# Kernel optimization log

Measured on AMD Instinct MI355X. Metric: run time of the kernel, lower is better.

The kernel has to match this reference:

```python
import jax, jax.numpy as jnp
import numpy as np

B, N, S, K = 8, 4096, 256, 128   # clouds, points/cloud, FPS samples (num_vote_test), neighbor cap
R = 0.2                           # ball-query radius
M = 45                            # FoldingNet grid side -> 45*45 = 2025 grid points


def _fps(pos):
    """Deterministic farthest point sampling of S points from pos [N,3] (start at index 0)."""
    n = pos.shape[0]
    big = jnp.finfo(pos.dtype).max

    def step(carry, _):
        mind, last = carry
        d = jnp.sum((pos - pos[last]) ** 2, axis=-1)
        mind = jnp.minimum(mind, d)
        nxt = jnp.argmax(mind).astype(jnp.int32)
        return (mind, nxt), nxt

    init = (jnp.full((n,), big, pos.dtype), jnp.int32(0))
    _, rest = jax.lax.scan(step, init, None, length=S - 1)
    return jnp.concatenate([jnp.zeros((1,), jnp.int32), rest])


def _forward(pos, Wt, bt, Wc1, bc1, Wc2, bc2, Wc3, bc3, We1, be1, We2, be2,
             Wf11, bf11, Wf12, bf12, Wf13, bf13, Wf21, bf21, Wf22, bf22, Wf23, bf23):
    lrelu = jax.nn.leaky_relu  # slope 0.01, matches torch LeakyReLU default
    # transformer: mlp([3,64]) -- BatchNorm at eval with default stats is identity
    x = lrelu(pos @ Wt + bt)                                  # [B,N,64]
    # FPS per cloud
    idx = jax.vmap(_fps)(pos)                                  # [B,S]
    new_pos = jnp.take_along_axis(pos, idx[..., None], axis=1)  # [B,S,3]
    # radius ball query: first K in-ball neighbors by index order (torch_cluster semantics)
    d2 = jnp.sum((new_pos[:, :, None, :] - pos[:, None, :, :]) ** 2, -1)  # [B,S,N]
    inball = d2 <= R * R
    keep = inball & (jnp.cumsum(inball, axis=-1) <= K)
    order = jnp.where(keep, jnp.arange(N)[None, None, :], N)
    nidx = jnp.sort(order, axis=-1)[..., :K]                   # [B,S,K]
    valid = nidx < N
    nsafe = jnp.minimum(nidx, N - 1)
    gather = jax.vmap(lambda a, i: a[i])
    xj = gather(x, nsafe)                                      # [B,S,K,64]
    pj = gather(pos, nsafe)                                    # [B,S,K,3]
    # PointConv: mlp(cat[x_j, pos_j - pos_i]) with max aggregation
    feat = jnp.concatenate([xj, pj - new_pos[:, :, None, :]], -1)  # [B,S,K,67]
    h = lrelu(feat @ Wc1 + bc1)
    h = lrelu(h @ Wc2 + bc2)
    h = lrelu(h @ Wc3 + bc3)                                   # [B,S,K,512]
    neg = jnp.finfo(h.dtype).min
    agg = jnp.max(jnp.where(valid[..., None], h, neg), axis=2)  # [B,S,512]
    # encoder mlp([515, 512, 2*bottleneck], last=True)
    e = lrelu(jnp.concatenate([agg, new_pos], -1) @ We1 + be1)
    e = e @ We2 + be2                                          # [B,S,2*bottleneck]
    mean, logvar = jnp.split(e, 2, axis=-1)
    std = jnp.exp(0.5 * logvar)
    # feature_selection (eval, rand=False): all S votes contribute; vote aggregation
    z = jnp.sum(mean / std, axis=1) / jnp.sum(1.0 / std, axis=1)  # [B,bottleneck]
    # FoldingNet decoder: 45x45 grid in [-0.3,0.3]^2, conv1x1 == last-dim linear
    g1 = np.linspace(-0.3, 0.3, M, dtype=np.float32)
    mg = np.meshgrid(g1, g1)
    grid = jnp.asarray(np.stack([mg[0].reshape(-1), mg[1].reshape(-1)], -1))  # [M*M,2]
    G = M * M
    code = jnp.broadcast_to(z[:, None, :], (z.shape[0], G, z.shape[1]))
    gb = jnp.broadcast_to(grid[None], (z.shape[0], G, 2))
    f = jnp.concatenate([code, gb], -1)                        # [B,G,bottleneck+2]
    f = jax.nn.relu(f @ Wf11 + bf11)
    f = jax.nn.relu(f @ Wf12 + bf12)
    f = f @ Wf13 + bf13                                        # [B,G,3]
    f2 = jnp.concatenate([code, f], -1)                        # [B,G,bottleneck+3]
    f2 = jax.nn.relu(f2 @ Wf21 + bf21)
    f2 = jax.nn.relu(f2 @ Wf22 + bf22)
    return f2 @ Wf23 + bf23                                    # [B,G,3]


_PARAM_SHAPES = [
    ("Wt", (3, 64)), ("bt", (64,)),
    ("Wc1", (67, 64)), ("bc1", (64,)),
    ("Wc2", (64, 128)), ("bc2", (128,)),
    ("Wc3", (128, 512)), ("bc3", (512,)),
    ("We1", (515, 512)), ("be1", (512,)),
    ("We2", (512, 2048)), ("be2", (2048,)),
    ("Wf11", (1026, 512)), ("bf11", (512,)),
    ("Wf12", (512, 512)), ("bf12", (512,)),
    ("Wf13", (512, 3)), ("bf13", (3,)),
    ("Wf21", (1027, 512)), ("bf21", (512,)),
    ("Wf22", (512, 512)), ("bf22", (512,)),
    ("Wf23", (512, 3)), ("bf23", (3,)),
]


def setup_inputs() -> dict:
    key = jax.random.key(0)
    inp = {"pos": jax.random.uniform(key, (B, N, 3), jnp.float32)}
    for i, (nm, sh) in enumerate(_PARAM_SHAPES):
        k = jax.random.fold_in(key, i + 1)
        fan_in = sh[0]
        inp[nm] = jax.random.normal(k, sh, jnp.float32) / np.sqrt(fan_in)
    return inp


def reference(pos, Wt, bt, Wc1, bc1, Wc2, bc2, Wc3, bc3, We1, be1, We2, be2,
              Wf11, bf11, Wf12, bf12, Wf13, bf13, Wf21, bf21, Wf22, bf22, Wf23, bf23):
    return _forward(pos, Wt, bt, Wc1, bc1, Wc2, bc2, Wc3, bc3, We1, be1, We2, be2,
                    Wf11, bf11, Wf12, bf12, Wf13, bf13, Wf21, bf21, Wf22, bf22, Wf23, bf23)
```

## Files before the change

kernel.cpp:

```cpp
#include <hip/hip_runtime.h>
#include <math.h>

#define BATCH 8
#define NPTS 4096
#define SSAMP 256
#define KNBR 128
#define GGRID 2025

typedef __attribute__((ext_vector_type(8))) short bf16x8;
typedef __attribute__((ext_vector_type(8))) unsigned short u16x8;
typedef __attribute__((ext_vector_type(4))) float f32x4;
#define MFMA16(a, b, c) __builtin_amdgcn_mfma_f32_16x16x32_bf16((a), (b), (c), 0, 0, 0)

__device__ __forceinline__ float lrelu01(float v) { return v > 0.f ? v : 0.01f * v; }
__device__ __forceinline__ unsigned short f2bf(float f) {
    unsigned u = __float_as_uint(f);
    unsigned r = (u + 0x7FFFu + ((u >> 16) & 1u)) >> 16;
    return (unsigned short)r;
}
__device__ __forceinline__ unsigned long long umax64(unsigned long long a, unsigned long long b) {
    return a > b ? a : b;
}

__global__ void preconv_kernel(const float* __restrict__ Wc1, const float* __restrict__ Wc2,
                               const float* __restrict__ Wc3, const float* __restrict__ We1,
                               const float* __restrict__ We2, const float* __restrict__ Wf12,
                               const float* __restrict__ Wf22,
                               unsigned short* __restrict__ W1T, unsigned short* __restrict__ W2T,
                               unsigned short* __restrict__ W3T, unsigned short* __restrict__ We1T,
                               unsigned short* __restrict__ We2T, unsigned short* __restrict__ Wf12T,
                               unsigned short* __restrict__ Wf22T) {
    int o = blockIdx.x * 256 + threadIdx.x;
    const int S1 = 6144, S2 = 8192, S3 = 65536, S4 = 294912, S5 = 1048576, S6 = 262144;
    if (o < S1) { int n = o / 96, k = o - n * 96; W1T[o] = f2bf(k < 67 ? Wc1[k * 64 + n] : 0.f); return; }
    o -= S1;
    if (o < S2) { int n = o >> 6, k = o & 63; W2T[o] = f2bf(Wc2[k * 128 + n]); return; }
    o -= S2;
    if (o < S3) { int n = o >> 7, k = o & 127; W3T[o] = f2bf(Wc3[k * 512 + n]); return; }
    o -= S3;
    if (o < S4) { int n = o / 576, k = o - n * 576; We1T[o] = f2bf(k < 515 ? We1[k * 512 + n] : 0.f); return; }
    o -= S4;
    if (o < S5) {
        int np = o >> 9, k = o & 511;
        int src = (np & 1) ? 1024 + (np >> 1) : (np >> 1);
        We2T[o] = f2bf(We2[(size_t)k * 2048 + src]);
        return;
    }
    o -= S5;
    if (o < S6) { int n = o >> 9, k = o & 511; Wf12T[o] = f2bf(Wf12[k * 512 + n]); return; }
    o -= S6;
    { int n = o >> 9, k = o & 511; Wf22T[o] = f2bf(Wf22[k * 512 + n]); }
}

__global__ void __launch_bounds__(256, 3) stage1_kernel(
    const float* __restrict__ pos, float* __restrict__ newpos, int* __restrict__ prog,
    const float* __restrict__ Wt, const float* __restrict__ bt,
    const unsigned short* __restrict__ W1T, const unsigned short* __restrict__ W2T,
    const unsigned short* __restrict__ W3T,
    const float* __restrict__ bc1, const float* __restrict__ bc2, const float* __restrict__ bc3,
    unsigned short* __restrict__ encin) {
    __shared__ __align__(16) unsigned char smem[53760];
    int blk = blockIdx.x, t = threadIdx.x;
    int wave = t >> 6, lane = t & 63;

    if (blk < 8) {
        float* pxs = (float*)smem;
        float* pys = (float*)(smem + 16384);
        float* pzs = (float*)(smem + 32768);
        float* npb = (float*)(smem + 49152);
        unsigned long long* rk = (unsigned long long*)(smem + 52224);
        int b = blk;
        const float* P = pos + (size_t)b * NPTS * 3;
        float* np = newpos + (size_t)b * SSAMP * 3;
        float px[16], py[16], pz[16], mind[16];
#pragma unroll
        for (int j = 0; j < 16; ++j) {
            int n = t + 256 * j;
            float X = P[n * 3 + 0], Y = P[n * 3 + 1], Z = P[n * 3 + 2];
            px[j] = X; py[j] = Y; pz[j] = Z;
            pxs[n] = X; pys[n] = Y; pzs[n] = Z;
            mind[j] = 3.402823466e+38f;
        }
        float cx = P[0], cy = P[1], cz = P[2];
        if (t == 0) { npb[0] = cx; npb[1] = cy; npb[2] = cz; }
        __syncthreads();
        for (int s = 1; s < SSAMP; ++s) {
            int p = s & 1;
            unsigned long long k[16];
#pragma unroll
            for (int j = 0; j < 16; ++j) {
                float dx = __fsub_rn(px[j], cx), dy = __fsub_rn(py[j], cy), dz = __fsub_rn(pz[j], cz);
// ... 14 lines not shown
                key = umax64(umax64(key, a), umax64(b2, c));
                a = __shfl_xor(key, 4, 64);
                b2 = __shfl_xor(key, 8, 64);
                c = __shfl_xor(key, 12, 64);
                key = umax64(umax64(key, a), umax64(b2, c));
                a = __shfl_xor(key, 16, 64);
                b2 = __shfl_xor(key, 32, 64);
                c = __shfl_xor(key, 48, 64);
                key = umax64(umax64(key, a), umax64(b2, c));
            }
            if (lane == 0) rk[p * 4 + wave] = key;
            __syncthreads();
            unsigned long long k0 = rk[p * 4 + 0], k1 = rk[p * 4 + 1];
            unsigned long long k2 = rk[p * 4 + 2], k3 = rk[p * 4 + 3];
            unsigned long long bk = umax64(umax64(k0, k1), umax64(k2, k3));
            int nx = (int)(~(unsigned)(bk & 0xFFFFFFFFull));
            cx = pxs[nx]; cy = pys[nx]; cz = pzs[nx];
            if (t == 0) {
                npb[s * 3 + 0] = cx;
                npb[s * 3 + 1] = cy;
                npb[s * 3 + 2] = cz;
            }
            if ((s & 7) == 7) {
                if (t < 24) np[(s - 7) * 3 + t] = npb[(s - 7) * 3 + t];
                if (t == 0) {
                    __threadfence();
                    __hip_atomic_store(&prog[b], s, __ATOMIC_RELAXED, __HIP_MEMORY_SCOPE_AGENT);
                }
            }
        }
        return;
    }

    unsigned short* featl = (unsigned short*)smem;
    unsigned short* h2    = (unsigned short*)smem;
    unsigned short* h1    = (unsigned short*)(smem + 34816);
    float* mred = (float*)(smem + 34816);
    int*   vld  = (int*)(smem + 53248);
    int*   wl   = (int*)smem;
    int*   cnt  = (int*)(smem + 2048);
    float* wtb  = (float*)(smem + 26624);

    int cons = blk - 8;
    int s = cons >> 3, b = cons & 7;
    int bs = b * 256 + s;
    int quad = lane >> 4, l16 = lane & 15;

    if (t == 0) {
        while (__hip_atomic_load(&prog[b], __ATOMIC_RELAXED, __HIP_MEMORY_SCOPE_AGENT) < s)
            __builtin_amdgcn_s_sleep(16);
    }
    __syncthreads();
    __threadfence();
    float q0 = newpos[(size_t)bs * 3 + 0];
    float q1 = newpos[(size_t)bs * 3 + 1];
    float q2 = newpos[(size_t)bs * 3 + 2];

    const float* P = pos + (size_t)b * NPTS * 3;
    {
        int base = 0;
        for (int c = 0; c < 16 && base < KNBR; ++c) {
            int n = wave * 1024 + c * 64 + lane;
            float dx = __fsub_rn(P[n * 3 + 0], q0);
            float dy = __fsub_rn(P[n * 3 + 1], q1);
            float dz = __fsub_rn(P[n * 3 + 2], q2);
            float d2 = __fadd_rn(__fadd_rn(__fmul_rn(dx, dx), __fmul_rn(dy, dy)), __fmul_rn(dz, dz));
            bool in = (d2 <= 0.04f);
            unsigned long long mask = __ballot(in);
            if (in) {
                int p = base + __popcll(mask & ((1ull << lane) - 1ull));
                if (p < KNBR) wl[wave * 128 + p] = n;
            }
            base += __popcll(mask);
        }
        if (lane == 0) cnt[wave] = base < KNBR ? base : KNBR;
    }
    __syncthreads();
    {
        int c0 = cnt[0], c1 = cnt[1], c2 = cnt[2], c3 = cnt[3];
        if (t < 128) {
            int idx = -1, r = t;
            if (r < c0) idx = wl[r];
            else {
// ... 143 lines not shown
            for (int nt = 0; nt < 8; ++nt) {
                bf16x8 bfr = *(const bf16x8*)(W3T + ((size_t)((c3 * 8 + nt) * 16 + l16)) * 128 + ks * 32 + quad * 8);
                acc[0][nt] = MFMA16(afr[0], bfr, acc[0][nt]);
                acc[1][nt] = MFMA16(afr[1], bfr, acc[1][nt]);
            }
        }
#pragma unroll
        for (int nt = 0; nt < 8; ++nt) {
            float vmax = -3.402823466e+38f;
#pragma unroll
            for (int i = 0; i < 2; ++i)
#pragma unroll
                for (int reg = 0; reg < 4; ++reg)
                    if (vbits & (1 << (i * 4 + reg))) vmax = fmaxf(vmax, acc[i][nt][reg]);
            vmax = fmaxf(vmax, __shfl_xor(vmax, 16));
            vmax = fmaxf(vmax, __shfl_xor(vmax, 32));
            if (lane < 16) mred[wave * 512 + (c3 * 8 + nt) * 16 + l16] = vmax;
        }
    }
    __syncthreads();
    unsigned short* erow = encin + (size_t)bs * 576;
    for (int c = t; c < 576; c += 256) {
        unsigned short v;
        if (c < 512) {
            float m4 = fmaxf(fmaxf(mred[c], mred[512 + c]), fmaxf(mred[1024 + c], mred[1536 + c]));
            v = f2bf(lrelu01(m4 + bc3[c]));
        } else if (c < 515) {
            v = f2bf(c == 512 ? q0 : (c == 513 ? q1 : q2));
        } else v = 0;
        erow[c] = v;
    }
}

__global__ void __launch_bounds__(256, 3) mfma_gemm(
    const unsigned short* __restrict__ A, const unsigned short* __restrict__ BT,
    const float* __restrict__ bias, unsigned short* __restrict__ outh,
    int M, int Ka, int Ncols, int act) {
    __shared__ __align__(16) unsigned short As[128 * 72];
    int t = threadIdx.x;
    int wave = t >> 6, lane = t & 63, quad = lane >> 4, l16 = lane & 15;
    int row0 = blockIdx.x * 128, col0 = blockIdx.y * 128;
    f32x4 acc[2][8];
#pragma unroll
    for (int i = 0; i < 2; ++i)
#pragma unroll
        for (int nt = 0; nt < 8; ++nt) acc[i][nt] = (f32x4){0.f, 0.f, 0.f, 0.f};
    int nk = Ka >> 6;
    int sr = t >> 1, sh = t & 1;
    int grow = row0 + sr; if (grow > M - 1) grow = M - 1;
    const unsigned short* Arow = A + (size_t)grow * Ka + sh * 32;
    for (int ks = 0; ks < nk; ++ks) {
        u16x8 av[4];
#pragma unroll
        for (int j = 0; j < 4; ++j) av[j] = *(const u16x8*)(Arow + ks * 64 + j * 8);
        __syncthreads();
#pragma unroll
        for (int j = 0; j < 4; ++j) *(u16x8*)&As[sr * 72 + sh * 32 + j * 8] = av[j];
        __syncthreads();
#pragma unroll
        for (int ks2 = 0; ks2 < 2; ++ks2) {
            bf16x8 afr[2];
            afr[0] = *(const bf16x8*)&As[((2 * wave) * 16 + l16) * 72 + ks2 * 32 + quad * 8];
            afr[1] = *(const bf16x8*)&As[((2 * wave + 1) * 16 + l16) * 72 + ks2 * 32 + quad * 8];
#pragma unroll
            for (int nt = 0; nt < 8; ++nt) {
                bf16x8 bfr = *(const bf16x8*)(BT + (size_t)(col0 + nt * 16 + l16) * Ka + ks * 64 + ks2 * 32 + quad * 8);
                acc[0][nt] = MFMA16(afr[0], bfr, acc[0][nt]);
                acc[1][nt] = MFMA16(afr[1], bfr, acc[1][nt]);
            }
        }
    }
#pragma unroll
    for (int i = 0; i < 2; ++i)
#pragma unroll
        for (int nt = 0; nt < 8; ++nt) {
            int col = col0 + nt * 16 + l16;
            float bv = bias[col];
#pragma unroll
            for (int reg = 0; reg < 4; ++reg) {
                int row = row0 + (2 * wave + i) * 16 + quad * 4 + reg;
                if (row < M) {
                    float v = acc[i][nt][reg] + bv;
                    if (act == 1) v = fmaxf(v, 0.f);
                    else if (act == 2) v = lrelu01(v);
                    outh[(size_t)row * Ncols + col] = f2bf(v);
                }
            }
        }
}

__global__ void __launch_bounds__(256, 3) e2v_kernel(
    const unsigned short* __restrict__ A, const unsigned short* __restrict__ BT,
    const float* __restrict__ be2, float* __restrict__ zacc) {
    __shared__ __align__(16) unsigned short As[128 * 72];
    int t = threadIdx.x;
    int wave = t >> 6, lane = t & 63, quad = lane >> 4, l16 = lane & 15;
    int row0 = blockIdx.x * 128, col0 = blockIdx.y * 128;
    f32x4 acc[2][8];
#pragma unroll
    for (int i = 0; i < 2; ++i)
#pragma unroll
        for (int nt = 0; nt < 8; ++nt) acc[i][nt] = (f32x4){0.f, 0.f, 0.f, 0.f};
    int sr = t >> 1, sh = t & 1;
    const unsigned short* Arow = A + (size_t)(row0 + sr) * 512 + sh * 32;
    for (int ks = 0; ks < 8; ++ks) {
        u16x8 av[4];
#pragma unroll
        for (int j = 0; j < 4; ++j) av[j] = *(const u16x8*)(Arow + ks * 64 + j * 8);
        __syncthreads();
#pragma unroll
        for (int j = 0; j < 4; ++j) *(u16x8*)&As[sr * 72 + sh * 32 + j * 8] = av[j];
        __syncthreads();
#pragma unroll
        for (int ks2 = 0; ks2 < 2; ++ks2) {
            bf16x8 afr[2];
            afr[0] = *(const bf16x8*)&As[((2 * wave) * 16 + l16) * 72 + ks2 * 32 + quad * 8];
            afr[1] = *(const bf16x8*)&As[((2 * wave + 1) * 16 + l16) * 72 + ks2 * 32 + quad * 8];
#pragma unroll
            for (int nt = 0; nt < 8; ++nt) {
                bf16x8 bfr = *(const bf16x8*)(BT + (size_t)(col0 + nt * 16 + l16) * 512 + ks * 64 + ks2 * 32 + quad * 8);
                acc[0][nt] = MFMA16(afr[0], bfr, acc[0][nt]);
                acc[1][nt] = MFMA16(afr[1], bfr, acc[1][nt]);
            }
        }
    }
    int b = row0 >> 8;
#pragma unroll
    for (int nt = 0; nt < 8; ++nt) {
        int colp = col0 + nt * 16 + l16;
        int c2 = colp >> 1;
        int srcc = (colp & 1) ? 1024 + c2 : c2;
        float bv = be2[srcc];
        float num = 0.f, den = 0.f;
#pragma unroll
        for (int i = 0; i < 2; ++i)
#pragma unroll
            for (int reg = 0; reg < 4; ++reg) {
                float val = acc[i][nt][reg] + bv;
                float par = __shfl_xor(val, 1, 64);
                float d = expf(-0.5f * par);
                num += val * d;
                den += d;
            }
        num += __shfl_xor(num, 16, 64); den += __shfl_xor(den, 16, 64);
        num += __shfl_xor(num, 32, 64); den += __shfl_xor(den, 32, 64);
        if (quad == 0 && !(l16 & 1)) {
            atomicAdd(&zacc[((b << 10) + c2) * 2 + 0], num);
            atomicAdd(&zacc[((b << 10) + c2) * 2 + 1], den);
        }
    }
}

__global__ void __launch_bounds__(256) ukern(const float* __restrict__ zacc,
                                             const float* __restrict__ Wf11, const float* __restrict__ bf11,
                                             const float* __restrict__ Wf21, const float* __restrict__ bf21,
                                             float* __restrict__ u1, float* __restrict__ u2) {
    __shared__ float zt[1024 * 8];
    __shared__ float red[4][64][8];
    const float* W = blockIdx.y ? Wf21 : Wf11;
    const float* bias = blockIdx.y ? bf21 : bf11;
    float* u = blockIdx.y ? u2 : u1;
    int t = threadIdx.x;
    const float2* za = (const float2*)zacc;
#pragma unroll
    for (int i = 0; i < 32; ++i) {
        int o = t + i * 256;
        float2 nd = za[o];
        zt[(o & 1023) * 8 + (o >> 10)] = nd.x / nd.y;
    }
    __syncthreads();
    int c64 = t & 63, kc = t >> 6;
    int co = blockIdx.x * 64 + c64;
    float acc[8];
#pragma unroll
    for (int r = 0; r < 8; ++r) acc[r] = 0.f;
    for (int i = 0; i < 256; ++i) {
        int ci = kc * 256 + i;
        float w = W[(size_t)ci * 512 + co];
        const float4* zp = (const float4*)&zt[ci * 8];
        float4 z0 = zp[0], z1 = zp[1];
        acc[0] = fmaf(z0.x, w, acc[0]); acc[1] = fmaf(z0.y, w, acc[1]);
        acc[2] = fmaf(z0.z, w, acc[2]); acc[3] = fmaf(z0.w, w, acc[3]);
        acc[4] = fmaf(z1.x, w, acc[4]); acc[5] = fmaf(z1.y, w, acc[5]);
        acc[6] = fmaf(z1.z, w, acc[6]); acc[7] = fmaf(z1.w, w, acc[7]);
    }
#pragma unroll
    for (int r = 0; r < 8; ++r) red[kc][c64][r] = acc[r];
    __syncthreads();
    if (kc == 0) {
#pragma unroll
        for (int r = 0; r < 8; ++r) {
            float v = red[0][c64][r] + red[1][c64][r] + red[2][c64][r] + red[3][c64][r] + bias[co];
            u[r * 512 + co] = v;
        }
    }
}

__global__ void __launch_bounds__(256, 3) foldfuse_kernel(
    const float* __restrict__ u, const float* __restrict__ Wfold, int nExtra, int mode,
    const unsigned short* __restrict__ WT, const float* __restrict__ bmid,
    const float* __restrict__ wout, const float* __restrict__ bout,
    const float* __restrict__ pts_in, float* __restrict__ outv) {
    __shared__ __align__(16) unsigned short As[128 * 72];
    __shared__ float sW[3][512];
    __shared__ float sU[2][512];
    __shared__ float sP[512 * 3];
    __shared__ float sB[512];
    __shared__ float sRC[128][4];
    int t = threadIdx.x, wave = t >> 6, lane = t & 63, quad = lane >> 4, l16 = lane & 15;
    int row0 = blockIdx.x * 128;
    int b0 = row0 / 2025;

    for (int idx = t; idx < 1536; idx += 256) {
        int r = idx >> 9, c = idx & 511;
        sW[r][c] = (r < nExtra) ? Wfold[(size_t)(1024 + r) * 512 + c] : 0.f;
    }
    for (int idx = t; idx < 1536; idx += 256) sP[idx] = wout[idx];
    for (int idx = t; idx < 1024; idx += 256) {
        int rb = idx >> 9;
        int bb = b0 + rb; if (bb > 7) bb = 7;
        sU[rb][idx & 511] = u[bb * 512 + (idx & 511)];
    }
    for (int idx = t; idx < 512; idx += 256) sB[idx] = bmid[idx];
    if (t < 128) {
        int rg = row0 + t; if (rg > 16199) rg = 16199;
        int b = rg / 2025, g = rg - b * 2025;
        if (mode == 0) {
            int i = g / 45, j = g - i * 45;
            sRC[t][0] = (j == 44) ? 0.3f : (float)(-0.3 + j * (0.6 / 44.0));
            sRC[t][1] = (i == 44) ? 0.3f : (float)(-0.3 + i * (0.6 / 44.0));
            sRC[t][2] = 0.f;
        } else {
            sRC[t][0] = pts_in[rg * 3 + 0];
            sRC[t][1] = pts_in[rg * 3 + 1];
            sRC[t][2] = pts_in[rg * 3 + 2];
        }
        sRC[t][3] = __int_as_float(b - b0);
    }
    __syncthreads();

    float proj[2][4][3];
#pragma unroll
    for (int i = 0; i < 2; ++i)
#pragma unroll
        for (int r = 0; r < 4; ++r) { proj[i][r][0] = 0.f; proj[i][r][1] = 0.f; proj[i][r][2] = 0.f; }

    int sr = t >> 1, sh = t & 1;
    for (int cc = 0; cc < 4; ++cc) {
        f32x4 acc[2][8];
#pragma unroll
        for (int i = 0; i < 2; ++i)
#pragma unroll
            for (int nt = 0; nt < 8; ++nt) acc[i][nt] = (f32x4){0.f, 0.f, 0.f, 0.f};
        for (int ks = 0; ks < 8; ++ks) {
            __syncthreads();
            {
                int ubi = __float_as_int(sRC[sr][3]);
                float r0 = sRC[sr][0], r1 = sRC[sr][1], r2 = sRC[sr][2];
                const float* up = sU[ubi];
                int cbase = ks * 64 + sh * 32;
#pragma unroll
                for (int g2 = 0; g2 < 16; ++g2) {
                    int c = cbase + g2 * 2;
                    float v0 = fmaf(r2, sW[2][c],     fmaf(r1, sW[1][c],     fmaf(r0, sW[0][c],     up[c])));
                    float v1 = fmaf(r2, sW[2][c + 1], fmaf(r1, sW[1][c + 1], fmaf(r0, sW[0][c + 1], up[c + 1])));
                    unsigned pk = (unsigned)f2bf(fmaxf(v0, 0.f)) | ((unsigned)f2bf(fmaxf(v1, 0.f)) << 16);
                    *(unsigned*)&As[sr * 72 + sh * 32 + g2 * 2] = pk;
                }
            }
            __syncthreads();
#pragma unroll
            for (int ks2 = 0; ks2 < 2; ++ks2) {
                bf16x8 afr0 = *(const bf16x8*)&As[((2 * wave) * 16 + l16) * 72 + ks2 * 32 + quad * 8];
                bf16x8 afr1 = *(const bf16x8*)&As[((2 * wave + 1) * 16 + l16) * 72 + ks2 * 32 + quad * 8];
#pragma unroll
                for (int nt = 0; nt < 8; ++nt) {
                    bf16x8 bfr = *(const bf16x8*)(WT + (size_t)(cc * 128 + nt * 16 + l16) * 512 + ks * 64 + ks2 * 32 + quad * 8);
                    acc[0][nt] = MFMA16(afr0, bfr, acc[0][nt]);
                    acc[1][nt] = MFMA16(afr1, bfr, acc[1][nt]);
                }
            }
        }
#pragma unroll
        for (int i = 0; i < 2; ++i)
#pragma unroll
            for (int nt = 0; nt < 8; ++nt) {
                int col = cc * 128 + nt * 16 + l16;
                float bv = sB[col];
                float w0 = sP[col * 3 + 0], w1 = sP[col * 3 + 1], w2 = sP[col * 3 + 2];
#pragma unroll
                for (int reg = 0; reg < 4; ++reg) {
                    float h = fmaxf(acc[i][nt][reg] + bv, 0.f);
                    proj[i][reg][0] = fmaf(h, w0, proj[i][reg][0]);
                    proj[i][reg][1] = fmaf(h, w1, proj[i][reg][1]);
                    proj[i][reg][2] = fmaf(h, w2, proj[i][reg][2]);
                }
            }
    }
    float o0 = bout[0], o1 = bout[1], o2 = bout[2];
#pragma unroll
    for (int i = 0; i < 2; ++i)
#pragma unroll
        for (int reg = 0; reg < 4; ++reg) {
            float p0 = proj[i][reg][0], p1 = proj[i][reg][1], p2 = proj[i][reg][2];
#pragma unroll
            for (int m = 1; m < 16; m <<= 1) {
                p0 += __shfl_xor(p0, m, 64);
                p1 += __shfl_xor(p1, m, 64);
                p2 += __shfl_xor(p2, m, 64);
            }
            if (l16 == 0) {
                int row = row0 + (2 * wave + i) * 16 + quad * 4 + reg;
                if (row < 16200) {
                    outv[row * 3 + 0] = p0 + o0;
                    outv[row * 3 + 1] = p1 + o1;
                    outv[row * 3 + 2] = p2 + o2;
                }
            }
        }
}

extern "C" void kernel_launch(void* const* d_in, const int* in_sizes, int n_in,
                              void* d_out, int out_size, void* d_ws, size_t ws_size,
                              hipStream_t stream) {
    const float* pos  = (const float*)d_in[0];
    const float* Wt   = (const float*)d_in[1];
    const float* bt   = (const float*)d_in[2];
    const float* Wc1  = (const float*)d_in[3];
    const float* bc1  = (const float*)d_in[4];
    const float* Wc2  = (const float*)d_in[5];
    const float* bc2  = (const float*)d_in[6];
    const float* Wc3  = (const float*)d_in[7];
    const float* bc3  = (const float*)d_in[8];
    const float* We1  = (const float*)d_in[9];
    const float* be1  = (const float*)d_in[10];
    const float* We2  = (const float*)d_in[11];
    const float* be2  = (const float*)d_in[12];
    const float* Wf11 = (const float*)d_in[13];
    const float* bf11 = (const float*)d_in[14];
    const float* Wf12 = (const float*)d_in[15];
    const float* bf12 = (const float*)d_in[16];
    const float* Wf13 = (const float*)d_in[17];
    const float* bf13 = (const float*)d_in[18];
    const float* Wf21 = (const float*)d_in[19];
    const float* bf21 = (const float*)d_in[20];
    const float* Wf22 = (const float*)d_in[21];
    const float* bf22 = (const float*)d_in[22];
    const float* Wf23 = (const float*)d_in[23];
    const float* bf23 = (const float*)d_in[24];
    float* out = (float*)d_out;

    float* wsf = (float*)d_ws;
    size_t off = 0;
    unsigned short* encinh= (unsigned short*)(wsf + off); off += 589824;
    unsigned short* e1h   = (unsigned short*)(wsf + off); off += 524288;
    float* zacc = wsf + off; off += 16384;
    float* u1   = wsf + off; off += 4096;
    float* u2   = wsf + off; off += 4096;
    float* pts  = wsf + off; off += 48600;
    float* newp = wsf + off; off += 6144;
    int*   prog = (int*)(wsf + off); off += 16;
    unsigned short* W1T   = (unsigned short*)(wsf + off); off += 3072;
    unsigned short* W2T   = (unsigned short*)(wsf + off); off += 4096;
    unsigned short* W3T   = (unsigned short*)(wsf + off); off += 32768;
    unsigned short* We1T  = (unsigned short*)(wsf + off); off += 147456;
    unsigned short* We2T  = (unsigned short*)(wsf + off); off += 524288;
    unsigned short* Wf12T = (unsigned short*)(wsf + off); off += 131072;
    unsigned short* Wf22T = (unsigned short*)(wsf + off); off += 131072;

    hipMemsetAsync(prog, 0xFF, 64, stream);
    hipMemsetAsync(zacc, 0x00, 16384 * 4, stream);
    preconv_kernel<<<7608, 256, 0, stream>>>(Wc1, Wc2, Wc3, We1, We2, Wf12, Wf22,
                                             W1T, W2T, W3T, We1T, We2T, Wf12T, Wf22T);
    stage1_kernel<<<2056, 256, 0, stream>>>(pos, newp, prog, Wt, bt, W1T, W2T, W3T,
                                            bc1, bc2, bc3, encinh);
    mfma_gemm<<<dim3(16, 4), 256, 0, stream>>>(encinh, We1T, be1, e1h, 2048, 576, 512, 2);
    e2v_kernel<<<dim3(16, 16), 256, 0, stream>>>(e1h, We2T, be2, zacc);
    ukern<<<dim3(8, 2), 256, 0, stream>>>(zacc, Wf11, bf11, Wf21, bf21, u1, u2);
    foldfuse_kernel<<<127, 256, 0, stream>>>(u1, Wf11, 2, 0, Wf12T, bf12, Wf13, bf13, pts, pts);
    foldfuse_kernel<<<127, 256, 0, stream>>>(u2, Wf21, 3, 1, Wf22T, bf22, Wf23, bf23, pts, out);
}
```

Baseline: 697.1 us.

## Fold weight preconversion into stage1 and fuse tail kernels with counters

Moves the bf16 weight transpose/convert work into extra blocks of the stage1 kernel so it overlaps with FPS, and consumer blocks spin on a counter until the conv weights are ready. The five tail kernels (encoder GEMMs, u projection, two folding stages) are merged into one persistent-style kernel whose blocks wait on per-row-block atomic counters instead of kernel boundaries. This removes several launch gaps and lets stages overlap. The cost is spin-wait dependencies that rely on block scheduling order and could deadlock or stall if producers are not resident.

```diff
diff --git a/kernel.cpp b/kernel.cpp
--- a/kernel.cpp
+++ b/kernel.cpp
@@ -21,42 +21,22 @@
 __device__ __forceinline__ unsigned long long umax64(unsigned long long a, unsigned long long b) {
     return a > b ? a : b;
 }
-
-__global__ void preconv_kernel(const float* __restrict__ Wc1, const float* __restrict__ Wc2,
-                               const float* __restrict__ Wc3, const float* __restrict__ We1,
-                               const float* __restrict__ We2, const float* __restrict__ Wf12,
-                               const float* __restrict__ Wf22,
-                               unsigned short* __restrict__ W1T, unsigned short* __restrict__ W2T,
-                               unsigned short* __restrict__ W3T, unsigned short* __restrict__ We1T,
-                               unsigned short* __restrict__ We2T, unsigned short* __restrict__ Wf12T,
-                               unsigned short* __restrict__ Wf22T) {
-    int o = blockIdx.x * 256 + threadIdx.x;
-    const int S1 = 6144, S2 = 8192, S3 = 65536, S4 = 294912, S5 = 1048576, S6 = 262144;
-    if (o < S1) { int n = o / 96, k = o - n * 96; W1T[o] = f2bf(k < 67 ? Wc1[k * 64 + n] : 0.f); return; }
-    o -= S1;
-    if (o < S2) { int n = o >> 6, k = o & 63; W2T[o] = f2bf(Wc2[k * 128 + n]); return; }
-    o -= S2;
-    if (o < S3) { int n = o >> 7, k = o & 127; W3T[o] = f2bf(Wc3[k * 512 + n]); return; }
-    o -= S3;
-    if (o < S4) { int n = o / 576, k = o - n * 576; We1T[o] = f2bf(k < 515 ? We1[k * 512 + n] : 0.f); return; }
-    o -= S4;
-    if (o < S5) {
-        int np = o >> 9, k = o & 511;
-        int src = (np & 1) ? 1024 + (np >> 1) : (np >> 1);
-        We2T[o] = f2bf(We2[(size_t)k * 2048 + src]);
-        return;
-    }
-    o -= S5;
-    if (o < S6) { int n = o >> 9, k = o & 511; Wf12T[o] = f2bf(Wf12[k * 512 + n]); return; }
-    o -= S6;
-    { int n = o >> 9, k = o & 511; Wf22T[o] = f2bf(Wf22[k * 512 + n]); }
+__device__ __forceinline__ void spin_ge(const int* p, int target) {
+    while (__hip_atomic_load(p, __ATOMIC_RELAXED, __HIP_MEMORY_SCOPE_AGENT) < target)
+        __builtin_amdgcn_s_sleep(16);
 }
 
 __global__ void __launch_bounds__(256, 3) stage1_kernel(
     const float* __restrict__ pos, float* __restrict__ newpos, int* __restrict__ prog,
+    int* __restrict__ cnts,
     const float* __restrict__ Wt, const float* __restrict__ bt,
-    const unsigned short* __restrict__ W1T, const unsigned short* __restrict__ W2T,
-    const unsigned short* __restrict__ W3T,
+    const float* __restrict__ Wc1, const float* __restrict__ Wc2, const float* __restrict__ Wc3,
+    const float* __restrict__ We1, const float* __restrict__ We2,
+    const float* __restrict__ Wf12, const float* __restrict__ Wf22,
+    unsigned short* __restrict__ W1T, unsigned short* __restrict__ W2T,
+    unsigned short* __restrict__ W3T, unsigned short* __restrict__ We1T,
+    unsigned short* __restrict__ We2T, unsigned short* __restrict__ Wf12T,
+    unsigned short* __restrict__ Wf22T,
     const float* __restrict__ bc1, const float* __restrict__ bc2, const float* __restrict__ bc3,
     unsigned short* __restrict__ encin) {
     __shared__ __align__(16) unsigned char smem[53760];
@@ -137,6 +117,39 @@
         return;
     }
 
+    if (blk < 959) {
+        int pb = blk - 8;
+        const int S1 = 6144, S2 = 8192, S3 = 65536, S4 = 294912, S5 = 1048576, S6 = 262144;
+#pragma unroll
+        for (int j = 0; j < 8; ++j) {
+            int o = pb * 2048 + t + j * 256;
+            int q = o;
+            if (q < S1) { int n = q / 96, k = q - n * 96; W1T[q] = f2bf(k < 67 ? Wc1[k * 64 + n] : 0.f); continue; }
+            q -= S1;
+            if (q < S2) { int n = q >> 6, k = q & 63; W2T[q] = f2bf(Wc2[k * 128 + n]); continue; }
+            q -= S2;
+            if (q < S3) { int n = q >> 7, k = q & 127; W3T[q] = f2bf(Wc3[k * 512 + n]); continue; }
+            q -= S3;
+            if (q < S4) { int n = q / 576, k = q - n * 576; We1T[q] = f2bf(k < 515 ? We1[k * 512 + n] : 0.f); continue; }
+            q -= S4;
+            if (q < S5) {
+                int np2 = q >> 9, k = q & 511;
+                int src = (np2 & 1) ? 1024 + (np2 >> 1) : (np2 >> 1);
+                We2T[q] = f2bf(We2[(size_t)k * 2048 + src]);
+                continue;
+            }
+            q -= S5;
+            if (q < S6) { int n = q >> 9, k = q & 511; Wf12T[q] = f2bf(Wf12[k * 512 + n]); continue; }
+            q -= S6;
+            { int n = q >> 9, k = q & 511; Wf22T[q] = f2bf(Wf22[k * 512 + n]); }
+        }
+        if (pb < 39) {
+            __syncthreads();
+            if (t == 0) { __threadfence(); atomicAdd(&cnts[19], 1); }
+        }
+        return;
+    }
+
     unsigned short* featl = (unsigned short*)smem;
     unsigned short* h2    = (unsigned short*)smem;
     unsigned short* h1    = (unsigned short*)(smem + 34816);
@@ -146,14 +159,14 @@
     int*   cnt  = (int*)(smem + 2048);
     float* wtb  = (float*)(smem + 26624);
 
-    int cons = blk - 8;
+    int cons = blk - 959;
     int s = cons >> 3, b = cons & 7;
     int bs = b * 256 + s;
     int quad = lane >> 4, l16 = lane & 15;
 
     if (t == 0) {
-        while (__hip_atomic_load(&prog[b], __ATOMIC_RELAXED, __HIP_MEMORY_SCOPE_AGENT) < s)
-            __builtin_amdgcn_s_sleep(16);
+        spin_ge(&prog[b], s);
+        spin_ge(&cnts[19], 39);
     }
     __syncthreads();
     __threadfence();
@@ -363,242 +376,53 @@
     }
 }
 
-__global__ void __launch_bounds__(256, 3) mfma_gemm(
-    const unsigned short* __restrict__ A, const unsigned short* __restrict__ BT,
-    const float* __restrict__ bias, unsigned short* __restrict__ outh,
-    int M, int Ka, int Ncols, int act) {
-    __shared__ __align__(16) unsigned short As[128 * 72];
-    int t = threadIdx.x;
+__global__ void __launch_bounds__(256, 2) tail_kernel(
+    const unsigned short* __restrict__ encinh, const unsigned short* __restrict__ We1T,
+    const float* __restrict__ be1, unsigned short* __restrict__ e1h,
+    const unsigned short* __restrict__ We2T, const float* __restrict__ be2,
+    float* __restrict__ zacc, int* __restrict__ cnts,
+    const float* __restrict__ Wf11, const float* __restrict__ bf11,
+    const float* __restrict__ Wf21, const float* __restrict__ bf21,
+    float* __restrict__ u1, float* __restrict__ u2,
+    const unsigned short* __restrict__ Wf12T, const float* __restrict__ bf12,
+    const float* __restrict__ Wf13, const float* __restrict__ bf13,
+    const unsigned short* __restrict__ Wf22T, const float* __restrict__ bf22,
+    const float* __restrict__ Wf23, const float* __restrict__ bf23,
+    float* __restrict__ pts, float* __restrict__ outv) {
+    __shared__ __align__(16) unsigned char smem[40960];
+    int blk = blockIdx.x, t = threadIdx.x;
     int wave = t >> 6, lane = t & 63, quad = lane >> 4, l16 = lane & 15;
-    int row0 = blockIdx.x * 128, col0 = blockIdx.y * 128;
-    f32x4 acc[2][8];
-#pragma unroll
-    for (int i = 0; i < 2; ++i)
-#pragma unroll
-        for (int nt = 0; nt < 8; ++nt) acc[i][nt] = (f32x4){0.f, 0.f, 0.f, 0.f};
-    int nk = Ka >> 6;
-    int sr = t >> 1, sh = t & 1;
-    int grow = row0 + sr; if (grow > M - 1) grow = M - 1;
-    const unsigned short* Arow = A + (size_t)grow * Ka + sh * 32;
-    for (int ks = 0; ks < nk; ++ks) {
-        u16x8 av[4];
-#pragma unroll
-        for (int j = 0; j < 4; ++j) av[j] = *(const u16x8*)(Arow + ks * 64 + j * 8);
-        __syncthreads();
-#pragma unroll
-        for (int j = 0; j < 4; ++j) *(u16x8*)&As[sr * 72 + sh * 32 + j * 8] = av[j];
-        __syncthreads();
-#pragma unroll
-        for (int ks2 = 0; ks2 < 2; ++ks2) {
-            bf16x8 afr[2];
-            afr[0] = *(const bf16x8*)&As[((2 * wave) * 16 + l16) * 72 + ks2 * 32 + quad * 8];
-            afr[1] = *(const bf16x8*)&As[((2 * wave + 1) * 16 + l16) * 72 + ks2 * 32 + quad * 8];
-#pragma unroll
-            for (int nt = 0; nt < 8; ++nt) {
-                bf16x8 bfr = *(const bf16x8*)(BT + (size_t)(col0 + nt * 16 + l16) * Ka + ks * 64 + ks2 * 32 + quad * 8);
-                acc[0][nt] = MFMA16(afr[0], bfr, acc[0][nt]);
-                acc[1][nt] = MFMA16(afr[1], bfr, acc[1][nt]);
-            }
-        }
-    }
-#pragma unroll
-    for (int i = 0; i < 2; ++i)
-#pragma unroll
-        for (int nt = 0; nt < 8; ++nt) {
-            int col = col0 + nt * 16 + l16;
-            float bv = bias[col];
-#pragma unroll
-            for (int reg = 0; reg < 4; ++reg) {
-                int row = row0 + (2 * wave + i) * 16 + quad * 4 + reg;
-                if (row < M) {
-                    float v = acc[i][nt][reg] + bv;
-                    if (act == 1) v = fmaxf(v, 0.f);
-                    else if (act == 2) v = lrelu01(v);
-                    outh[(size_t)row * Ncols + col] = f2bf(v);
-                }
-            }
-        }
-}
-
-__global__ void __launch_bounds__(256, 3) e2v_kernel(
-    const unsigned short* __restrict__ A, const unsigned short* __restrict__ BT,
-    const float* __restrict__ be2, float* __restrict__ zacc) {
-    __shared__ __align__(16) unsigned short As[128 * 72];
-    int t = threadIdx.x;
-    int wave = t >> 6, lane = t & 63, quad = lane >> 4, l16 = lane & 15;
-    int row0 = blockIdx.x * 128, col0 = blockIdx.y * 128;
-    f32x4 acc[2][8];
-#pragma unroll
-    for (int i = 0; i < 2; ++i)
-#pragma unroll
-        for (int nt = 0; nt < 8; ++nt) acc[i][nt] = (f32x4){0.f, 0.f, 0.f, 0.f};
-    int sr = t >> 1, sh = t & 1;
-    const unsigned short* Arow = A + (size_t)(row0 + sr) * 512 + sh * 32;
-    for (int ks = 0; ks < 8; ++ks) {
-        u16x8 av[4];
-#pragma unroll
-        for (int j = 0; j < 4; ++j) av[j] = *(const u16x8*)(Arow + ks * 64 + j * 8);
-        __syncthreads();
-#pragma unroll
-        for (int j = 0; j < 4; ++j) *(u16x8*)&As[sr * 72 + sh * 32 + j * 8] = av[j];
-        __syncthreads();
-#pragma unroll
-        for (int ks2 = 0; ks2 < 2; ++ks2) {
-            bf16x8 afr[2];
-            afr[0] = *(const bf16x8*)&As[((2 * wave) * 16 + l16) * 72 + ks2 * 32 + quad * 8];
-            afr[1] = *(const bf16x8*)&As[((2 * wave + 1) * 16 + l16) * 72 + ks2 * 32 + quad * 8];
-#pragma unroll
-            for (int nt = 0; nt < 8; ++nt) {
-                bf16x8 bfr = *(const bf16x8*)(BT + (size_t)(col0 + nt * 16 + l16) * 512 + ks * 64 + ks2 * 32 + quad * 8);
-                acc[0][nt] = MFMA16(afr[0], bfr, acc[0][nt]);
-                acc[1][nt] = MFMA16(afr[1], bfr, acc[1][nt]);
-            }
-        }
-    }
-    int b = row0 >> 8;
-#pragma unroll
-    for (int nt = 0; nt < 8; ++nt) {
-        int colp = col0 + nt * 16 + l16;
-        int c2 = colp >> 1;
-        int srcc = (colp & 1) ? 1024 + c2 : c2;
-        float bv = be2[srcc];
-        float num = 0.f, den = 0.f;
+
+    if (blk < 320) {
+        unsigned short* As = (unsigned short*)smem;
+        bool is_e1 = blk < 64;
+        int rb, cb;
+        const unsigned short* A;
+        const unsigned short* BT;
+        int Ka;
+        if (is_e1) { rb = blk >> 2; cb = blk & 3; A = encinh; BT = We1T; Ka = 576; }
+        else {
+            int j = blk - 64; rb = j >> 4; cb = j & 15; A = e1h; BT = We2T; Ka = 512;
+            if (t == 0) spin_ge(&cnts[rb], 4);
+            __syncthreads();
+            __threadfence();
+        }
+        int row0 = rb * 128, col0 = cb * 128;
+        f32x4 acc[2][8];
 #pragma unroll
         for (int i = 0; i < 2; ++i)
 #pragma unroll
-            for (int reg = 0; reg < 4; ++reg) {
-                float val = acc[i][nt][reg] + bv;
-                float par = __shfl_xor(val, 1, 64);
-                float d = expf(-0.5f * par);
-                num += val * d;
-                den += d;
-            }
-        num += __shfl_xor(num, 16, 64); den += __shfl_xor(den, 16, 64);
-        num += __shfl_xor(num, 32, 64); den += __shfl_xor(den, 32, 64);
-        if (quad == 0 && !(l16 & 1)) {
-            atomicAdd(&zacc[((b << 10) + c2) * 2 + 0], num);
-            atomicAdd(&zacc[((b << 10) + c2) * 2 + 1], den);
-        }
-    }
-}
-
-__global__ void __launch_bounds__(256) ukern(const float* __restrict__ zacc,
-                                             const float* __restrict__ Wf11, const float* __restrict__ bf11,
-                                             const float* __restrict__ Wf21, const float* __restrict__ bf21,
-                                             float* __restrict__ u1, float* __restrict__ u2) {
-    __shared__ float zt[1024 * 8];
-    __shared__ float red[4][64][8];
-    const float* W = blockIdx.y ? Wf21 : Wf11;
-    const float* bias = blockIdx.y ? bf21 : bf11;
-    float* u = blockIdx.y ? u2 : u1;
-    int t = threadIdx.x;
-    const float2* za = (const float2*)zacc;
-#pragma unroll
-    for (int i = 0; i < 32; ++i) {
-        int o = t + i * 256;
-        float2 nd = za[o];
-        zt[(o & 1023) * 8 + (o >> 10)] = nd.x / nd.y;
-    }
-    __syncthreads();
-    int c64 = t & 63, kc = t >> 6;
-    int co = blockIdx.x * 64 + c64;
-    float acc[8];
-#pragma unroll
-    for (int r = 0; r < 8; ++r) acc[r] = 0.f;
-    for (int i = 0; i < 256; ++i) {
-        int ci = kc * 256 + i;
-        float w = W[(size_t)ci * 512 + co];
-        const float4* zp = (const float4*)&zt[ci * 8];
-        float4 z0 = zp[0], z1 = zp[1];
-        acc[0] = fmaf(z0.x, w, acc[0]); acc[1] = fmaf(z0.y, w, acc[1]);
-        acc[2] = fmaf(z0.z, w, acc[2]); acc[3] = fmaf(z0.w, w, acc[3]);
-        acc[4] = fmaf(z1.x, w, acc[4]); acc[5] = fmaf(z1.y, w, acc[5]);
-        acc[6] = fmaf(z1.z, w, acc[6]); acc[7] = fmaf(z1.w, w, acc[7]);
-    }
-#pragma unroll
-    for (int r = 0; r < 8; ++r) red[kc][c64][r] = acc[r];
-    __syncthreads();
-    if (kc == 0) {
-#pragma unroll
-        for (int r = 0; r < 8; ++r) {
-            float v = red[0][c64][r] + red[1][c64][r] + red[2][c64][r] + red[3][c64][r] + bias[co];
-            u[r * 512 + co] = v;
-        }
-    }
-}
-
-__global__ void __launch_bounds__(256, 3) foldfuse_kernel(
-    const float* __restrict__ u, const float* __restrict__ Wfold, int nExtra, int mode,
-    const unsigned short* __restrict__ WT, const float* __restrict__ bmid,
-    const float* __restrict__ wout, const float* __restrict__ bout,
-    const float* __restrict__ pts_in, float* __restrict__ outv) {
-    __shared__ __align__(16) unsigned short As[128 * 72];
-    __shared__ float sW[3][512];
-    __shared__ float sU[2][512];
-    __shared__ float sP[512 * 3];
-    __shared__ float sB[512];
-    __shared__ float sRC[128][4];
-    int t = threadIdx.x, wave = t >> 6, lane = t & 63, quad = lane >> 4, l16 = lane & 15;
-    int row0 = blockIdx.x * 128;
-    int b0 = row0 / 2025;
-
-    for (int idx = t; idx < 1536; idx += 256) {
-        int r = idx >> 9, c = idx & 511;
-        sW[r][c] = (r < nExtra) ? Wfold[(size_t)(1024 + r) * 512 + c] : 0.f;
-    }
-    for (int idx = t; idx < 1536; idx += 256) sP[idx] = wout[idx];
-    for (int idx = t; idx < 1024; idx += 256) {
-        int rb = idx >> 9;
-        int bb = b0 + rb; if (bb > 7) bb = 7;
-        sU[rb][idx & 511] = u[bb * 512 + (idx & 511)];
-    }
-    for (int idx = t; idx < 512; idx += 256) sB[idx] = bmid[idx];
-    if (t < 128) {
-        int rg = row0 + t; if (rg > 16199) rg = 16199;
-        int b = rg / 2025, g = rg - b * 2025;
-        if (mode == 0) {
-            int i = g / 45, j = g - i * 45;
-            sRC[t][0] = (j == 44) ? 0.3f : (float)(-0.3 + j * (0.6 / 44.0));
-            sRC[t][1] = (i == 44) ? 0.3f : (float)(-0.3 + i * (0.6 / 44.0));
-            sRC[t][2] = 0.f;
-        } else {
-            sRC[t][0] = pts_in[rg * 3 + 0];
-            sRC[t][1] = pts_in[rg * 3 + 1];
-            sRC[t][2] = pts_in[rg * 3 + 2];
-        }
-        sRC[t][3] = __int_as_float(b - b0);
-    }
-    __syncthreads();
-
-    float proj[2][4][3];
-#pragma unroll
-    for (int i = 0; i < 2; ++i)
-#pragma unroll
-        for (int r = 0; r < 4; ++r) { proj[i][r][0] = 0.f; proj[i][r][1] = 0.f; proj[i][r][2] = 0.f; }
-
-    int sr = t >> 1, sh = t & 1;
-    for (int cc = 0; cc < 4; ++cc) {
-        f32x4 acc[2][8];
-#pragma unroll
-        for (int i = 0; i < 2; ++i)
-#pragma unroll
             for (int nt = 0; nt < 8; ++nt) acc[i][nt] = (f32x4){0.f, 0.f, 0.f, 0.f};
-        for (int ks = 0; ks < 8; ++ks) {
+        int nk = Ka >> 6;
+        int sr = t >> 1, sh = t & 1;
+        const unsigned short* Arow = A + (size_t)(row0 + sr) * Ka + sh * 32;
+        for (int ks = 0; ks < nk; ++ks) {
+            u16x8 av[4];
+#pragma unroll
+            for (int j = 0; j < 4; ++j) av[j] = *(const u16x8*)(Arow + ks * 64 + j * 8);
             __syncthreads();
-            {
-                int ubi = __float_as_int(sRC[sr][3]);
-                float r0 = sRC[sr][0], r1 = sRC[sr][1], r2 = sRC[sr][2];
-                const float* up = sU[ubi];
-                int cbase = ks * 64 + sh * 32;
-#pragma unroll
-                for (int g2 = 0; g2 < 16; ++g2) {
-                    int c = cbase + g2 * 2;
-                    float v0 = fmaf(r2, sW[2][c],     fmaf(r1, sW[1][c],     fmaf(r0, sW[0][c],     up[c])));
-                    float v1 = fmaf(r2, sW[2][c + 1], fmaf(r1, sW[1][c + 1], fmaf(r0, sW[0][c + 1], up[c + 1])));
-                    unsigned pk = (unsigned)f2bf(fmaxf(v0, 0.f)) | ((unsigned)f2bf(fmaxf(v1, 0.f)) << 16);
-                    *(unsigned*)&As[sr * 72 + sh * 32 + g2 * 2] = pk;
-                }
-            }
+#pragma unroll
+            for (int j = 0; j < 4; ++j) *(u16x8*)&As[sr * 72 + sh * 32 + j * 8] = av[j];
             __syncthreads();
 #pragma unroll
             for (int ks2 = 0; ks2 < 2; ++ks2) {
@@ -606,49 +430,248 @@
                 bf16x8 afr1 = *(const bf16x8*)&As[((2 * wave + 1) * 16 + l16) * 72 + ks2 * 32 + quad * 8];
 #pragma unroll
                 for (int nt = 0; nt < 8; ++nt) {
-                    bf16x8 bfr = *(const bf16x8*)(WT + (size_t)(cc * 128 + nt * 16 + l16) * 512 + ks * 64 + ks2 * 32 + quad * 8);
+                    bf16x8 bfr = *(const bf16x8*)(BT + (size_t)(col0 + nt * 16 + l16) * Ka + ks * 64 + ks2 * 32 + quad * 8);
                     acc[0][nt] = MFMA16(afr0, bfr, acc[0][nt]);
                     acc[1][nt] = MFMA16(afr1, bfr, acc[1][nt]);
                 }
             }
         }
+        if (is_e1) {
+#pragma unroll
+            for (int i = 0; i < 2; ++i)
+#pragma unroll
+                for (int nt = 0; nt < 8; ++nt) {
+                    int col = col0 + nt * 16 + l16;
+                    float bv = be1[col];
+#pragma unroll
+                    for (int reg = 0; reg < 4; ++reg) {
+                        int row = row0 + (2 * wave + i) * 16 + quad * 4 + reg;
+                        e1h[(size_t)row * 512 + col] = f2bf(lrelu01(acc[i][nt][reg] + bv));
+                    }
+                }
+            __syncthreads();
+            if (t == 0) { __threadfence(); atomicAdd(&cnts[rb], 1); }
+        } else {
+            int b = row0 >> 8;
+#pragma unroll
+            for (int nt = 0; nt < 8; ++nt) {
+                int colp = col0 + nt * 16 + l16;
+                int c2 = colp >> 1;
+                int srcc = (colp & 1) ? 1024 + c2 : c2;
+                float bv = be2[srcc];
+                float num = 0.f, den = 0.f;
+#pragma unroll
+                for (int i = 0; i < 2; ++i)
+#pragma unroll
+                    for (int reg = 0; reg < 4; ++reg) {
+                        float val = acc[i][nt][reg] + bv;
+                        float par = __shfl_xor(val, 1, 64);
+                        float d = expf(-0.5f * par);
+                        num += val * d;
+                        den += d;
+                    }
+                num += __shfl_xor(num, 16, 64); den += __shfl_xor(den, 16, 64);
+                num += __shfl_xor(num, 32, 64); den += __shfl_xor(den, 32, 64);
+                if (quad == 0 && !(l16 & 1)) {
+                    atomicAdd(&zacc[((b << 10) + c2) * 2 + 0], num);
+                    atomicAdd(&zacc[((b << 10) + c2) * 2 + 1], den);
+                }
+            }
+            __syncthreads();
+            if (t == 0) { __threadfence(); atomicAdd(&cnts[16], 1); }
+        }
+        return;
+    }
+
+    if (blk < 336) {
+        float* zt = (float*)smem;
+        float* red = (float*)(smem + 32768);
+        int j = blk - 320;
+        int dec = j >> 3, cb = j & 7;
+        const float* W = dec ? Wf21 : Wf11;
+        const float* bias = dec ? bf21 : bf11;
+        float* u = dec ? u2 : u1;
+        if (t == 0) spin_ge(&cnts[16], 256);
+        __syncthreads();
+        __threadfence();
+        const float2* za = (const float2*)zacc;
+#pragma unroll
+        for (int i = 0; i < 32; ++i) {
+            int o = t + i * 256;
+            float2 nd = za[o];
+            zt[(o & 1023) * 8 + (o >> 10)] = nd.x / nd.y;
+        }
+        __syncthreads();
+        int c64 = t & 63, kc = t >> 6;
+        int co = cb * 64 + c64;
+        float acc[8];
+#pragma unroll
+        for (int r = 0; r < 8; ++r) acc[r] = 0.f;
+        for (int i = 0; i < 256; ++i) {
+            int ci = kc * 256 + i;
+            float w = W[(size_t)ci * 512 + co];
+            const float4* zp = (const float4*)&zt[ci * 8];
+            float4 z0 = zp[0], z1 = zp[1];
+            acc[0] = fmaf(z0.x, w, acc[0]); acc[1] = fmaf(z0.y, w, acc[1]);
+            acc[2] = fmaf(z0.z, w, acc[2]); acc[3] = fmaf(z0.w, w, acc[3]);
+            acc[4] = fmaf(z1.x, w, acc[4]); acc[5] = fmaf(z1.y, w, acc[5]);
+            acc[6] = fmaf(z1.z, w, acc[6]); acc[7] = fmaf(z1.w, w, acc[7]);
+        }
+#pragma unroll
+        for (int r = 0; r < 8; ++r) red[(kc * 64 + c64) * 8 + r] = acc[r];
+        __syncthreads();
+        if (kc == 0) {
+#pragma unroll
+            for (int r = 0; r < 8; ++r) {
+                float v = red[(0 * 64 + c64) * 8 + r] + red[(1 * 64 + c64) * 8 + r]
+                        + red[(2 * 64 + c64) * 8 + r] + red[(3 * 64 + c64) * 8 + r] + bias[co];
+                u[r * 512 + co] = v;
+            }
+        }
+        __syncthreads();
+        if (t == 0) { __threadfence(); atomicAdd(&cnts[17 + dec], 1); }
+        return;
+    }
+
+    {
+        unsigned short* As = (unsigned short*)smem;
+        float* sW = (float*)(smem + 18432);
+        float* sU = (float*)(smem + 24576);
+        float* sP = (float*)(smem + 28672);
+        float* sB = (float*)(smem + 34816);
+        float* sRC = (float*)(smem + 36864);
+        int dec = blk < 463 ? 0 : 1;
+        int j = blk - (dec ? 463 : 336);
+        const float* u = dec ? u2 : u1;
+        const float* Wfold = dec ? Wf21 : Wf11;
+        int nExtra = dec ? 3 : 2;
+        const unsigned short* WT = dec ? Wf22T : Wf12T;
+        const float* bmid = dec ? bf22 : bf12;
+        const float* wout = dec ? Wf23 : Wf13;
+        const float* bout = dec ? bf23 : bf13;
+        float* ov = dec ? outv : pts;
+        int row0 = j * 128;
+        int b0 = row0 / 2025;
+
+        if (t == 0) {
+            spin_ge(&cnts[17 + dec], 8);
+            if (dec) spin_ge(&cnts[20 + j], 1);
+        }
+        __syncthreads();
+        __threadfence();
+
+        for (int idx = t; idx < 1536; idx += 256) {
+            int r = idx >> 9, c = idx & 511;
+            sW[r * 512 + c] = (r < nExtra) ? Wfold[(size_t)(1024 + r) * 512 + c] : 0.f;
+        }
+        for (int idx = t; idx < 1536; idx += 256) sP[idx] = wout[idx];
+        for (int idx = t; idx < 1024; idx += 256) {
+            int rb = idx >> 9;
+            int bb = b0 + rb; if (bb > 7) bb = 7;
+            sU[rb * 512 + (idx & 511)] = u[bb * 512 + (idx & 511)];
+        }
+        for (int idx = t; idx < 512; idx += 256) sB[idx] = bmid[idx];
+        if (t < 128) {
+            int rg = row0 + t; if (rg > 16199) rg = 16199;
+            int b = rg / 2025, g = rg - b * 2025;
+            if (dec == 0) {
+                int i = g / 45, jj = g - i * 45;
+                sRC[t * 4 + 0] = (jj == 44) ? 0.3f : (float)(-0.3 + jj * (0.6 / 44.0));
+                sRC[t * 4 + 1] = (i == 44) ? 0.3f : (float)(-0.3 + i * (0.6 / 44.0));
+                sRC[t * 4 + 2] = 0.f;
+            } else {
+                sRC[t * 4 + 0] = pts[rg * 3 + 0];
+                sRC[t * 4 + 1] = pts[rg * 3 + 1];
+                sRC[t * 4 + 2] = pts[rg * 3 + 2];
+            }
+            sRC[t * 4 + 3] = __int_as_float(b - b0);
+        }
+        __syncthreads();
+
+        float proj[2][4][3];
 #pragma unroll
         for (int i = 0; i < 2; ++i)
 #pragma unroll
-            for (int nt = 0; nt < 8; ++nt) {
-                int col = cc * 128 + nt * 16 + l16;
-                float bv = sB[col];
-                float w0 = sP[col * 3 + 0], w1 = sP[col * 3 + 1], w2 = sP[col * 3 + 2];
-#pragma unroll
-                for (int reg = 0; reg < 4; ++reg) {
-                    float h = fmaxf(acc[i][nt][reg] + bv, 0.f);
-                    proj[i][reg][0] = fmaf(h, w0, proj[i][reg][0]);
-                    proj[i][reg][1] = fmaf(h, w1, proj[i][reg][1]);
-                    proj[i][reg][2] = fmaf(h, w2, proj[i][reg][2]);
-                }
-            }
-    }
-    float o0 = bout[0], o1 = bout[1], o2 = bout[2];
-#pragma unroll
-    for (int i = 0; i < 2; ++i)
-#pragma unroll
-        for (int reg = 0; reg < 4; ++reg) {
-            float p0 = proj[i][reg][0], p1 = proj[i][reg][1], p2 = proj[i][reg][2];
-#pragma unroll
-            for (int m = 1; m < 16; m <<= 1) {
-                p0 += __shfl_xor(p0, m, 64);
-                p1 += __shfl_xor(p1, m, 64);
-                p2 += __shfl_xor(p2, m, 64);
-            }
-            if (l16 == 0) {
-                int row = row0 + (2 * wave + i) * 16 + quad * 4 + reg;
-                if (row < 16200) {
-                    outv[row * 3 + 0] = p0 + o0;
-                    outv[row * 3 + 1] = p1 + o1;
-                    outv[row * 3 + 2] = p2 + o2;
-                }
-            }
-        }
+            for (int r = 0; r < 4; ++r) { proj[i][r][0] = 0.f; proj[i][r][1] = 0.f; proj[i][r][2] = 0.f; }
+
+        int sr = t >> 1, sh = t & 1;
+        for (int cc = 0; cc < 4; ++cc) {
+            f32x4 acc[2][8];
+#pragma unroll
+            for (int i = 0; i < 2; ++i)
+#pragma unroll
+                for (int nt = 0; nt < 8; ++nt) acc[i][nt] = (f32x4){0.f, 0.f, 0.f, 0.f};
+            for (int ks = 0; ks < 8; ++ks) {
+                __syncthreads();
+                {
+                    int ubi = __float_as_int(sRC[sr * 4 + 3]);
+                    float r0 = sRC[sr * 4 + 0], r1 = sRC[sr * 4 + 1], r2 = sRC[sr * 4 + 2];
+                    const float* up = sU + ubi * 512;
+                    int cbase = ks * 64 + sh * 32;
+#pragma unroll
+                    for (int g2 = 0; g2 < 16; ++g2) {
+                        int c = cbase + g2 * 2;
+                        float v0 = fmaf(r2, sW[1024 + c],     fmaf(r1, sW[512 + c],     fmaf(r0, sW[c],     up[c])));
+                        float v1 = fmaf(r2, sW[1024 + c + 1], fmaf(r1, sW[512 + c + 1], fmaf(r0, sW[c + 1], up[c + 1])));
+                        unsigned pk = (unsigned)f2bf(fmaxf(v0, 0.f)) | ((unsigned)f2bf(fmaxf(v1, 0.f)) << 16);
+                        *(unsigned*)&As[sr * 72 + sh * 32 + g2 * 2] = pk;
+                    }
+                }
+                __syncthreads();
+#pragma unroll
+                for (int ks2 = 0; ks2 < 2; ++ks2) {
+                    bf16x8 afr0 = *(const bf16x8*)&As[((2 * wave) * 16 + l16) * 72 + ks2 * 32 + quad * 8];
+                    bf16x8 afr1 = *(const bf16x8*)&As[((2 * wave + 1) * 16 + l16) * 72 + ks2 * 32 + quad * 8];
+#pragma unroll
+                    for (int nt = 0; nt < 8; ++nt) {
+                        bf16x8 bfr = *(const bf16x8*)(WT + (size_t)(cc * 128 + nt * 16 + l16) * 512 + ks * 64 + ks2 * 32 + quad * 8);
+                        acc[0][nt] = MFMA16(afr0, bfr, acc[0][nt]);
+                        acc[1][nt] = MFMA16(afr1, bfr, acc[1][nt]);
+                    }
+                }
+            }
+#pragma unroll
+            for (int i = 0; i < 2; ++i)
+#pragma unroll
+                for (int nt = 0; nt < 8; ++nt) {
+                    int col = cc * 128 + nt * 16 + l16;
+                    float bv = sB[col];
+                    float w0 = sP[col * 3 + 0], w1 = sP[col * 3 + 1], w2 = sP[col * 3 + 2];
+#pragma unroll
+                    for (int reg = 0; reg < 4; ++reg) {
+                        float h = fmaxf(acc[i][nt][reg] + bv, 0.f);
+                        proj[i][reg][0] = fmaf(h, w0, proj[i][reg][0]);
+                        proj[i][reg][1] = fmaf(h, w1, proj[i][reg][1]);
+                        proj[i][reg][2] = fmaf(h, w2, proj[i][reg][2]);
+                    }
+                }
+        }
+        float o0 = bout[0], o1 = bout[1], o2 = bout[2];
+#pragma unroll
+        for (int i = 0; i < 2; ++i)
+#pragma unroll
+            for (int reg = 0; reg < 4; ++reg) {
+                float p0 = proj[i][reg][0], p1 = proj[i][reg][1], p2 = proj[i][reg][2];
+#pragma unroll
+                for (int m = 1; m < 16; m <<= 1) {
+                    p0 += __shfl_xor(p0, m, 64);
+                    p1 += __shfl_xor(p1, m, 64);
+                    p2 += __shfl_xor(p2, m, 64);
+                }
+                if (l16 == 0) {
+                    int row = row0 + (2 * wave + i) * 16 + quad * 4 + reg;
+                    if (row < 16200) {
+                        ov[row * 3 + 0] = p0 + o0;
+                        ov[row * 3 + 1] = p1 + o1;
+                        ov[row * 3 + 2] = p2 + o2;
+                    }
+                }
+            }
+        if (dec == 0) {
+            __syncthreads();
+            if (t == 0) { __threadfence(); atomicAdd(&cnts[20 + j], 1); }
+        }
+    }
 }
 
 extern "C" void kernel_launch(void* const* d_in, const int* in_sizes, int n_in,
@@ -691,6 +714,7 @@
     float* pts  = wsf + off; off += 48600;
     float* newp = wsf + off; off += 6144;
     int*   prog = (int*)(wsf + off); off += 16;
+    int*   cnts = (int*)(wsf + off); off += 256;
     unsigned short* W1T   = (unsigned short*)(wsf + off); off += 3072;
     unsigned short* W2T   = (unsigned short*)(wsf + off); off += 4096;
     unsigned short* W3T   = (unsigned short*)(wsf + off); off += 32768;
@@ -700,14 +724,14 @@
     unsigned short* Wf22T = (unsigned short*)(wsf + off); off += 131072;
 
     hipMemsetAsync(prog, 0xFF, 64, stream);
+    hipMemsetAsync(cnts, 0x00, 1024, stream);
     hipMemsetAsync(zacc, 0x00, 16384 * 4, stream);
-    preconv_kernel<<<7608, 256, 0, stream>>>(Wc1, Wc2, Wc3, We1, We2, Wf12, Wf22,
-                                             W1T, W2T, W3T, We1T, We2T, Wf12T, Wf22T);
-    stage1_kernel<<<2056, 256, 0, stream>>>(pos, newp, prog, Wt, bt, W1T, W2T, W3T,
+    stage1_kernel<<<3007, 256, 0, stream>>>(pos, newp, prog, cnts, Wt, bt,
+                                            Wc1, Wc2, Wc3, We1, We2, Wf12, Wf22,
+                                            W1T, W2T, W3T, We1T, We2T, Wf12T, Wf22T,
                                             bc1, bc2, bc3, encinh);
-    mfma_gemm<<<dim3(16, 4), 256, 0, stream>>>(encinh, We1T, be1, e1h, 2048, 576, 512, 2);
-    e2v_kernel<<<dim3(16, 16), 256, 0, stream>>>(e1h, We2T, be2, zacc);
-    ukern<<<dim3(8, 2), 256, 0, stream>>>(zacc, Wf11, bf11, Wf21, bf21, u1, u2);
-    foldfuse_kernel<<<127, 256, 0, stream>>>(u1, Wf11, 2, 0, Wf12T, bf12, Wf13, bf13, pts, pts);
-    foldfuse_kernel<<<127, 256, 0, stream>>>(u2, Wf21, 3, 1, Wf22T, bf22, Wf23, bf23, pts, out);
+    tail_kernel<<<590, 256, 0, stream>>>(encinh, We1T, be1, e1h, We2T, be2, zacc, cnts,
+                                         Wf11, bf11, Wf21, bf21, u1, u2,
+                                         Wf12T, bf12, Wf13, bf13,
+                                         Wf22T, bf22, Wf23, bf23, pts, out);
 }
```

Measured after the change: 770.8 us. 1.11x slower.
